# Optimization experiments

Hardware: AMD Instinct MI355X
Metric: run time of the kernel (lower is better)

The kernel has to match this reference:

```python
import jax, jax.numpy as jnp
import numpy as np

N = 50000       # nodes
E = 800000      # edges (avg degree 16)
IN_DIM = 256
OUT_DIM = 64
NEG_SLOPE = 0.01  # F.leaky_relu default


def setup_inputs() -> dict:
    key = jax.random.key(0)
    k1, k2, k3, k4, k5 = jax.random.split(key, 5)
    features = jax.random.normal(k1, (N, IN_DIM), dtype=jnp.float32)
    # xavier-normal-ish scaling for weights
    W = jax.random.normal(k2, (IN_DIM, OUT_DIM), dtype=jnp.float32) / np.sqrt(IN_DIM)
    a = jax.random.normal(k3, (2 * OUT_DIM,), dtype=jnp.float32) / np.sqrt(2 * OUT_DIM)
    src = jax.random.randint(k4, (E,), 0, N)
    dst = jax.random.randint(k5, (E,), 0, N)
    return {"features": features, "W": W, "a": a, "src": src, "dst": dst}


def reference(features, W, a, src, dst):
    # z = fc(dropout(features)); dropout p=0 / eval -> identity
    z = features @ W                               # [N, D]
    # attn_fc([z_src || z_dst]) == z_src @ a_l + z_dst @ a_r
    el = z @ a[:OUT_DIM]                           # [N]
    er = z @ a[OUT_DIM:]                           # [N]
    e = jax.nn.leaky_relu(el[src] + er[dst], NEG_SLOPE)  # [E]
    # segment softmax over incoming edges of each destination node
    m = jax.ops.segment_max(e, dst, num_segments=N)      # [N]
    ex = jnp.exp(e - m[dst])                              # [E]
    denom = jax.ops.segment_sum(ex, dst, num_segments=N)  # [N]
    safe_denom = jnp.where(denom == 0, 1.0, denom)
    alpha = ex / safe_denom[dst]                           # [E]
    # weighted aggregation of source features
    h = jax.ops.segment_sum(alpha[:, None] * z[src], dst, num_segments=N)  # [N, D]
    return jax.nn.elu(h)
```

## Files before the change

### kernel.cpp

```cpp
#include <hip/hip_runtime.h>
#include <math.h>
#include <stdint.h>


constexpr int IN_D   = 256;
constexpr int OUT_D  = 64;
constexpr int NBLK   = 256;
constexpr int NBMAX  = 1024;
constexpr int CAPE   = 4096;
constexpr int FWAVES = 16;

typedef _Float16 f16x8 __attribute__((ext_vector_type(8)));
typedef float    f32x4 __attribute__((ext_vector_type(4)));

__device__ __forceinline__ void gload_lds16(const void* g, void* l) {
    __builtin_amdgcn_global_load_lds(
        (const __attribute__((address_space(1))) uint32_t*)g,
        (__attribute__((address_space(3))) uint32_t*)l, 16, 0, 0);
}


__global__ __launch_bounds__(256) void k_count(const int* __restrict__ dst,
                                               int* __restrict__ blkcnt,
                                               int* __restrict__ cursor,
                                               int E, int nb, int chunk) {
    __shared__ int cnt[NBMAX];
    const int b = blockIdx.x, tid = threadIdx.x;
    if (b == 0 && tid == 0) *cursor = 0;
    for (int i = tid; i < nb; i += 256) cnt[i] = 0;
    __syncthreads();
    const int lo = b * chunk;
    const int hi = (lo + chunk < E) ? lo + chunk : E;
    const int nv = (hi - lo) & ~3;
    for (int e = lo + tid * 4; e < lo + nv; e += 1024) {
        int4 d4 = *(const int4*)&dst[e];
        atomicAdd(&cnt[d4.x >> 6], 1);
        atomicAdd(&cnt[d4.y >> 6], 1);
        atomicAdd(&cnt[d4.z >> 6], 1);
        atomicAdd(&cnt[d4.w >> 6], 1);
    }
    for (int e = lo + nv + tid; e < hi; e += 256) atomicAdd(&cnt[dst[e] >> 6], 1);
    __syncthreads();
    for (int i = tid; i < nb; i += 256) blkcnt[(size_t)b * NBMAX + i] = cnt[i];
}

__global__ __launch_bounds__(256) void k_bsum(int* __restrict__ blkcnt,
                                              int* __restrict__ total,
                                              int* __restrict__ bbase,
                                              int* __restrict__ cursor, int nb) {
    const int j = blockIdx.x * 256 + threadIdx.x;
    const int lane = threadIdx.x & 63;
    int run = 0;
    if (j < nb) {
        #pragma unroll 8
        for (int b = 0; b < NBLK; ++b) {
            int v = blkcnt[(size_t)b * NBMAX + j];
            blkcnt[(size_t)b * NBMAX + j] = run;
            run += v;
        }
    }
    int incl = run;
    #pragma unroll
    for (int ofs = 1; ofs < 64; ofs <<= 1) {
        int u = __shfl_up(incl, ofs, 64);
        if (lane >= ofs) incl += u;
    }
    int base = 0;
    if (lane == 63) base = atomicAdd(cursor, incl);
    base = __shfl(base, 63, 64);
    if (j < nb) { total[j] = run; bbase[j] = base + incl - run; }
}

__global__ __launch_bounds__(256) void k_bin(const int* __restrict__ dst,
                                             const int* __restrict__ src,
                                             const int* __restrict__ blkcnt,
                                             const int* __restrict__ bbase,
                                             uint32_t* __restrict__ binned,
                                             int E, int nb, int chunk) {
    __shared__ int cur[NBMAX];
    const int b = blockIdx.x, tid = threadIdx.x;
    for (int i = tid; i < nb; i += 256)
        cur[i] = bbase[i] + blkcnt[(size_t)b * NBMAX + i];
    __syncthreads();
    const int lo = b * chunk;
    const int hi = (lo + chunk < E) ? lo + chunk : E;
    const int nv = (hi - lo) & ~3;
    for (int e = lo + tid * 4; e < lo + nv; e += 1024) {
        int4 d4 = *(const int4*)&dst[e];
        int4 s4 = *(const int4*)&src[e];
        int p;
        p = atomicAdd(&cur[d4.x >> 6], 1); binned[p] = ((uint32_t)d4.x << 16) | (uint32_t)s4.x;
        p = atomicAdd(&cur[d4.y >> 6], 1); binned[p] = ((uint32_t)d4.y << 16) | (uint32_t)s4.y;
        p = atomicAdd(&cur[d4.z >> 6], 1); binned[p] = ((uint32_t)d4.z << 16) | (uint32_t)s4.z;
        p = atomicAdd(&cur[d4.w >> 6], 1); binned[p] = ((uint32_t)d4.w << 16) | (uint32_t)s4.w;
    }
    for (int e = lo + nv + tid; e < hi; e += 256) {
        const uint32_t d = (uint32_t)dst[e];
        const int pos = atomicAdd(&cur[d >> 6], 1);
        binned[pos] = (d << 16) | (uint32_t)src[e];
    }
}


__global__ void k_wconv(const float* __restrict__ W, _Float16* __restrict__ Wf) {
    int t = blockIdx.x * 256 + threadIdx.x;
    int j    = t & 7;
    int lane = (t >> 3) & 63;
    int ct   = (t >> 9) & 3;
    int kc   = t >> 11;
    int k = kc * 32 + (lane >> 4) * 8 + j;
    int c = ct * 16 + (lane & 15);
    Wf[t] = (_Float16)W[k * OUT_D + c];
}

__global__ __launch_bounds__(256) void k_gemmf16(
        const float* __restrict__ feat, const _Float16* __restrict__ Wf,
        const float* __restrict__ a,
        _Float16* __restrict__ z, float* __restrict__ el, float* __restrict__ er,
        int n)
{
    __shared__ __align__(16) _Float16 WfL[IN_D * OUT_D];

    const int tid  = threadIdx.x;
    const int lane = tid & 63;
    const int wv   = tid >> 6;
    const int row0 = blockIdx.x * 64 + wv * 16;
    const int kg   = lane >> 4;

    int gr = row0 + (lane & 15); if (gr > n - 1) gr = n - 1;
    const float* frow = feat + (size_t)gr * IN_D;
    float4 r0[8], r1[8];
    #pragma unroll
    for (int kc = 0; kc < 8; ++kc) {
        const float4* fp = (const float4*)(frow + kc * 32 + kg * 8);
        r0[kc] = fp[0];
        r1[kc] = fp[1];
    }

    #pragma unroll
    for (int i = 0; i < 8; ++i) {
        const char* gsrc = (const char*)Wf + (size_t)(i * 256 + tid) * 16;
        char* ldst = (char*)WfL + (size_t)(i * 256 + wv * 64) * 16;
        gload_lds16(gsrc, ldst);
    }
    __syncthreads();

    f32x4 acc[4];
    #pragma unroll
    for (int ct = 0; ct < 4; ++ct) acc[ct] = (f32x4){0.f, 0.f, 0.f, 0.f};

    #pragma unroll
    for (int kc = 0; kc < 8; ++kc) {
        f16x8 af;
        af[0] = (_Float16)r0[kc].x; af[1] = (_Float16)r0[kc].y;
        af[2] = (_Float16)r0[kc].z; af[3] = (_Float16)r0[kc].w;
        af[4] = (_Float16)r1[kc].x; af[5] = (_Float16)r1[kc].y;
        af[6] = (_Float16)r1[kc].z; af[7] = (_Float16)r1[kc].w;
        #pragma unroll
        for (int ct = 0; ct < 4; ++ct) {
            f16x8 bf = *(const f16x8*)&WfL[((kc * 4 + ct) * 64 + lane) * 8];
            acc[ct] = __builtin_amdgcn_mfma_f32_16x16x32_f16(af, bf, acc[ct], 0, 0, 0);
        }
    }

    const int col = lane & 15;
    float av[4], bv[4];
    #pragma unroll
    for (int ct = 0; ct < 4; ++ct) {
        av[ct] = a[ct * 16 + col];
        bv[ct] = a[OUT_D + ct * 16 + col];
    }
    #pragma unroll
    for (int i = 0; i < 4; ++i) {
        const int r = row0 + (lane >> 4) * 4 + i;
        float vl = 0.f, vr = 0.f;
        #pragma unroll
        for (int ct = 0; ct < 4; ++ct) {
            float zv = acc[ct][i];
            if (r < n) z[(size_t)r * OUT_D + ct * 16 + col] = (_Float16)zv;
            vl = fmaf(zv, av[ct], vl);
            vr = fmaf(zv, bv[ct], vr);
        }
        #pragma unroll
        for (int msk = 8; msk >= 1; msk >>= 1) {
            vl += __shfl_xor(vl, msk, 64);
            vr += __shfl_xor(vr, msk, 64);
        }
        if (col == 0 && r < n) { el[r] = vl; er[r] = vr; }
    }
}

__global__ __launch_bounds__(1024) void k_fagg(
        const uint32_t* __restrict__ binned, const int* __restrict__ bbase,
        const int* __restrict__ total,
        const _Float16* __restrict__ z, const float* __restrict__ el,
        const float* __restrict__ er, float* __restrict__ out, int n)
{
    __shared__ uint32_t pr[CAPE];
    __shared__ uint16_t adjs[CAPE];
    __shared__ int fcnt[64], foff[64], fcur[64];
    __shared__ float exs[FWAVES][64];

    const int j   = blockIdx.x, tid = threadIdx.x;
    const int lane = tid & 63;
    const int wv   = tid >> 6;
    const int ebase = bbase[j];
    int ecnt = total[j]; if (ecnt > CAPE) ecnt = CAPE;

    for (int i = tid; i < ecnt; i += 1024) pr[i] = binned[ebase + i];
    if (tid < 64) { fcnt[tid] = 0; fcur[tid] = 0; }
    __syncthreads();
    for (int i = tid; i < ecnt; i += 1024)
        atomicAdd(&fcnt[(pr[i] >> 16) & 63], 1);
    __syncthreads();
    if (tid < 64) {
        const int v = fcnt[tid];
        int incl = v;
        #pragma unroll
        for (int ofs = 1; ofs < 64; ofs <<= 1) {
            int u = __shfl_up(incl, ofs, 64);
            if (tid >= ofs) incl += u;
        }
        foff[tid] = incl - v;
    }
    __syncthreads();
    for (int i = tid; i < ecnt; i += 1024) {
        const uint32_t u = pr[i];
        const int ld = (u >> 16) & 63;
        const int r = atomicAdd(&fcur[ld], 1);
        adjs[foff[ld] + r] = (uint16_t)(u & 0xFFFFu);
    }
    __syncthreads();

    #pragma unroll
    for (int t = 0; t < 64 / FWAVES; ++t) {
        const int ld = wv * (64 / FWAVES) + t;
        const int d = j * 64 + ld;
        if (d >= n) continue;
        const int deg = fcnt[ld];
        const int sb  = foff[ld];
        const float erd = er[d];

        float m = -INFINITY, den = 0.f, acc = 0.f;
        for (int b0 = 0; b0 < deg; b0 += 64) {
            const int i = b0 + lane;
            float lgv = -INFINITY;
            if (i < deg) {
                const int s = adjs[sb + i];
                const float x = el[s] + erd;
                lgv = x > 0.f ? x : 0.01f * x;
            }
            float cm = lgv;
            #pragma unroll
            for (int msk = 32; msk >= 1; msk >>= 1) cm = fmaxf(cm, __shfl_xor(cm, msk, 64));
            const float newm = fmaxf(m, cm);
            const float ex = (i < deg) ? __expf(lgv - newm) : 0.f;
            exs[wv][lane] = ex;
            float sum = ex;
            #pragma unroll
            for (int msk = 32; msk >= 1; msk >>= 1) sum += __shfl_xor(sum, msk, 64);
            const float scale = __expf(m - newm);
            den = den * scale + sum;
            acc *= scale;
            m = newm;
            asm volatile("s_waitcnt lgkmcnt(0)" ::: "memory");

            const int cd = (deg - b0 < 64) ? deg - b0 : 64;
            #pragma unroll 8
            for (int q = 0; q < cd; ++q) {
                const float wq = exs[wv][q];
                const int   sq = adjs[sb + b0 + q];
                acc = fmaf(wq, (float)z[(size_t)sq * OUT_D + lane], acc);
            }
        }
        const float h = (deg > 0) ? acc / den : 0.f;
        out[(size_t)d * OUT_D + lane] = h > 0.f ? h : expm1f(h);
    }
}

extern "C" void kernel_launch(void* const* d_in, const int* in_sizes, int n_in,
                              void* d_out, int out_size, void* d_ws, size_t ws_size,
                              hipStream_t stream) {
    const float* feat = (const float*)d_in[0];
    const float* W    = (const float*)d_in[1];
    const float* a    = (const float*)d_in[2];
    const int*   src  = (const int*)d_in[3];
    const int*   dst  = (const int*)d_in[4];
    const int n = in_sizes[0] / IN_D;
    const int E = in_sizes[3];
    float* out = (float*)d_out;

    const int nb = (n + 63) >> 6;
    const int chunk = (((E + NBLK - 1) / NBLK) + 3) & ~3;

    char* ws = (char*)d_ws;
    _Float16* z_h = (_Float16*)ws;    ws += (size_t)n * OUT_D * 2;
    float* el = (float*)ws;           ws += (size_t)n * 4;
    float* er = (float*)ws;           ws += (size_t)n * 4;
    int*  total = (int*)ws;           ws += (size_t)NBMAX * 4;
    int*  bbase = (int*)ws;           ws += (size_t)NBMAX * 4;
    int*  cursor = (int*)ws;          ws += 16;
    int*  blkcnt = (int*)ws;          ws += (size_t)NBLK * NBMAX * 4;
    uint32_t* binned = (uint32_t*)ws; ws += (size_t)E * 4;
    _Float16* Wf = (_Float16*)ws;

    k_count<<<NBLK, 256, 0, stream>>>(dst, blkcnt, cursor, E, nb, chunk);
    k_bsum<<<(nb + 255) / 256, 256, 0, stream>>>(blkcnt, total, bbase, cursor, nb);
    k_bin<<<NBLK, 256, 0, stream>>>(dst, src, blkcnt, bbase, binned, E, nb, chunk);
    k_wconv<<<IN_D * OUT_D / 256, 256, 0, stream>>>(W, Wf);
    k_gemmf16<<<(n + 63) / 64, 256, 0, stream>>>(feat, Wf, a, z_h, el, er, n);
    k_fagg<<<nb, 1024, 0, stream>>>(binned, bbase, total, z_h, el, er, out, n);
}
```

Before: 165.8 us.

## Vectorize edge gather in aggregation: 4 edges per wave step, 8-byte loads

The aggregation loop now splits each 64-lane wave into four 16-lane groups. Each group handles a different edge, and each lane loads 4 half-precision features with one 8-byte load, so the loop runs a quarter as many iterations. Partial sums are combined with cross-lane shuffles, and the output is written as float4. Per-bin edge ranges are padded to multiples of 4, which lets the binned edge list be copied into shared memory with 16-byte vector loads. This costs extra workspace and adds a final reduction step.

```diff
diff --git a/kernel.cpp b/kernel.cpp
--- a/kernel.cpp
+++ b/kernel.cpp
@@ -59,7 +59,8 @@
             run += v;
         }
     }
-    int incl = run;
+    const int runp = (run + 3) & ~3;
+    int incl = runp;
     #pragma unroll
     for (int ofs = 1; ofs < 64; ofs <<= 1) {
         int u = __shfl_up(incl, ofs, 64);
@@ -68,7 +69,7 @@
     int base = 0;
     if (lane == 63) base = atomicAdd(cursor, incl);
     base = __shfl(base, 63, 64);
-    if (j < nb) { total[j] = run; bbase[j] = base + incl - run; }
+    if (j < nb) { total[j] = run; bbase[j] = base + incl - runp; }
 }
 
 __global__ __launch_bounds__(256) void k_bin(const int* __restrict__ dst,
@@ -196,8 +197,8 @@
         const _Float16* __restrict__ z, const float* __restrict__ el,
         const float* __restrict__ er, float* __restrict__ out, int n)
 {
-    __shared__ uint32_t pr[CAPE];
-    __shared__ uint16_t adjs[CAPE];
+    __shared__ __align__(16) uint32_t pr[CAPE];
+    __shared__ uint16_t adjs[CAPE + 4];
     __shared__ int fcnt[64], foff[64], fcur[64];
     __shared__ float exs[FWAVES][64];
 
@@ -207,7 +208,9 @@
     const int ebase = bbase[j];
     int ecnt = total[j]; if (ecnt > CAPE) ecnt = CAPE;
 
-    for (int i = tid; i < ecnt; i += 1024) pr[i] = binned[ebase + i];
+    const int nv4 = (ecnt + 3) >> 2;
+    for (int i = tid; i < nv4; i += 1024)
+        *(uint4*)&pr[i * 4] = *(const uint4*)&binned[ebase + i * 4];
     if (tid < 64) { fcnt[tid] = 0; fcur[tid] = 0; }
     __syncthreads();
     for (int i = tid; i < ecnt; i += 1024)
@@ -230,7 +233,11 @@
         const int r = atomicAdd(&fcur[ld], 1);
         adjs[foff[ld] + r] = (uint16_t)(u & 0xFFFFu);
     }
-    __syncthreads();
+    if (tid < 4) adjs[ecnt + tid] = 0;
+    __syncthreads();
+
+    const int sub = lane >> 4;
+    const int qc  = lane & 15;
 
     #pragma unroll
     for (int t = 0; t < 64 / FWAVES; ++t) {
@@ -241,7 +248,8 @@
         const int sb  = foff[ld];
         const float erd = er[d];
 
-        float m = -INFINITY, den = 0.f, acc = 0.f;
+        float m = -INFINITY, den = 0.f;
+        float4 acc = {0.f, 0.f, 0.f, 0.f};
         for (int b0 = 0; b0 < deg; b0 += 64) {
             const int i = b0 + lane;
             float lgv = -INFINITY;
@@ -261,20 +269,42 @@
             for (int msk = 32; msk >= 1; msk >>= 1) sum += __shfl_xor(sum, msk, 64);
             const float scale = __expf(m - newm);
             den = den * scale + sum;
-            acc *= scale;
+            acc.x *= scale; acc.y *= scale; acc.z *= scale; acc.w *= scale;
             m = newm;
             asm volatile("s_waitcnt lgkmcnt(0)" ::: "memory");
 
-            const int cd = (deg - b0 < 64) ? deg - b0 : 64;
-            #pragma unroll 8
-            for (int q = 0; q < cd; ++q) {
-                const float wq = exs[wv][q];
-                const int   sq = adjs[sb + b0 + q];
-                acc = fmaf(wq, (float)z[(size_t)sq * OUT_D + lane], acc);
+            const int cd  = (deg - b0 < 64) ? deg - b0 : 64;
+            const int nit = (cd + 3) >> 2;
+            for (int q = 0; q < nit; ++q) {
+                const int idx = 4 * q + sub;
+                const float wq = exs[wv][idx];
+                const int   sq = adjs[sb + b0 + idx];
+                const _Float16* zp = &z[(size_t)sq * OUT_D + qc * 4];
+                uint2 v = *(const uint2*)zp;
+                const _Float16* hf = (const _Float16*)&v;
+                acc.x = fmaf(wq, (float)hf[0], acc.x);
+                acc.y = fmaf(wq, (float)hf[1], acc.y);
+                acc.z = fmaf(wq, (float)hf[2], acc.z);
+                acc.w = fmaf(wq, (float)hf[3], acc.w);
             }
         }
-        const float h = (deg > 0) ? acc / den : 0.f;
-        out[(size_t)d * OUT_D + lane] = h > 0.f ? h : expm1f(h);
+        #pragma unroll
+        for (int msk = 16; msk <= 32; msk <<= 1) {
+            acc.x += __shfl_xor(acc.x, msk, 64);
+            acc.y += __shfl_xor(acc.y, msk, 64);
+            acc.z += __shfl_xor(acc.z, msk, 64);
+            acc.w += __shfl_xor(acc.w, msk, 64);
+        }
+        if (sub == 0) {
+            const float inv = (deg > 0) ? 1.f / den : 0.f;
+            float4 h;
+            h.x = acc.x * inv; h.y = acc.y * inv; h.z = acc.z * inv; h.w = acc.w * inv;
+            h.x = h.x > 0.f ? h.x : expm1f(h.x);
+            h.y = h.y > 0.f ? h.y : expm1f(h.y);
+            h.z = h.z > 0.f ? h.z : expm1f(h.z);
+            h.w = h.w > 0.f ? h.w : expm1f(h.w);
+            *(float4*)&out[(size_t)d * OUT_D + qc * 4] = h;
+        }
     }
 }
 
@@ -301,7 +331,7 @@
     int*  bbase = (int*)ws;           ws += (size_t)NBMAX * 4;
     int*  cursor = (int*)ws;          ws += 16;
     int*  blkcnt = (int*)ws;          ws += (size_t)NBLK * NBMAX * 4;
-    uint32_t* binned = (uint32_t*)ws; ws += (size_t)E * 4;
+    uint32_t* binned = (uint32_t*)ws; ws += ((size_t)E + 4 * NBMAX) * 4;
     _Float16* Wf = (_Float16*)ws;
 
     k_count<<<NBLK, 256, 0, stream>>>(dst, blkcnt, cursor, E, nb, chunk);
```

Result: no change. 166.4 us (+0.4%).
